# Performance work log

Measured on AMD Instinct MI355X. Metric: run time of the kernel, lower is better.

Reference implementation:

```python
import jax, jax.numpy as jnp
import numpy as np

NUM_ITERATIONS = 3


def squash(t, axis=-1):
    # scale * t / sqrt(||t||^2), scale = ||t||^2 / (1 + ||t||^2)
    sq = jnp.sum(t * t, axis=axis, keepdims=True)
    return t * (sq / ((1.0 + sq) * jnp.sqrt(sq)))


def setup_inputs() -> dict:
    key = jax.random.key(0)
    k1, k2 = jax.random.split(key)
    B, I, D = 512, 1152, 8   # batch, in_capsules, in_dim
    O, E = 10, 16            # out_capsules, out_dim
    x = jax.random.normal(k1, (B, I, D), dtype=jnp.float32)
    route_weights = jax.random.normal(k2, (O, I, D, E), dtype=jnp.float32)
    return {"x": x, "route_weights": route_weights}


def reference(x, route_weights):
    # priors: [O, B, I, E]  (torch version carries an extra singleton dim 3,
    # which only broadcasts; math is identical)
    priors = jnp.einsum('bid,oide->obie', x, route_weights)
    # logits broadcast over out_dim in the torch code (delta has keepdim=1 on
    # the last axis), so a [O, B, I, 1] logit tensor is exactly equivalent.
    logits = jnp.zeros(priors.shape[:3] + (1,), dtype=priors.dtype)
    outputs = None
    for it in range(NUM_ITERATIONS):
        probs = jax.nn.softmax(logits, axis=2)            # over in_capsules
        s = jnp.sum(probs * priors, axis=2, keepdims=True)  # [O, B, 1, E]
        outputs = squash(s, axis=-1)
        if it != NUM_ITERATIONS - 1:
            delta = jnp.sum(priors * outputs, axis=-1, keepdims=True)  # [O,B,I,1]
            logits = logits + delta
    # match torch output shape [out_capsules, batch, 1, 1, out_dim]
    return outputs[:, :, :, None, :]
```

## Files before the change

kernel.cpp:

```cpp
#include <hip/hip_runtime.h>

#define BATCH 512
#define NI 1152
#define ND 8
#define NO 10
#define NE 16

constexpr int THREADS = 512;
constexpr int WAVES   = THREADS / 64;
constexpr int QUADS   = THREADS / 4;
constexpr int ITEMS   = NI / QUADS;
constexpr int BB      = 2;
constexpr int BPG     = BATCH / BB;


__device__ __forceinline__ unsigned int bf16_rne(float f) {
    const unsigned int u = __builtin_bit_cast(unsigned int, f);
    return (u + 0x7fffu + ((u >> 16) & 1u)) >> 16;
}
__device__ __forceinline__ float bf_lo(unsigned int u) {
    return __builtin_bit_cast(float, u << 16);
}
__device__ __forceinline__ float bf_hi(unsigned int u) {
    return __builtin_bit_cast(float, u & 0xffff0000u);
}

__global__ __launch_bounds__(THREADS, 4)
void caps_routing(const float* __restrict__ x,
                  const float* __restrict__ Wt,
                  float* __restrict__ out)
{
    const int o  = blockIdx.x / BPG;
    const int b0 = (blockIdx.x % BPG) * BB;

    __shared__ __align__(16) unsigned int pl[BB][NI][NE / 2];
    __shared__ __align__(16) float red[BB][WAVES * 16];
    __shared__ float sv[BB][16];
    __shared__ float rsum[BB][WAVES];

    const int t    = threadIdx.x;
    const int lane = t & 63;
    const int w    = t >> 6;
    const int e4   = t & 3;
    const int iq   = t >> 2;

    const float* xb = x  + (size_t)b0 * (NI * ND);
    const float* Wo = Wt + (size_t)o * ((size_t)NI * ND * NE);

    float lg[BB][ITEMS];
    float4 acc[BB];
#pragma unroll
    for (int bb = 0; bb < BB; ++bb) acc[bb] = make_float4(0.f, 0.f, 0.f, 0.f);

#pragma unroll
    for (int k = 0; k < ITEMS; ++k) {
        const int i = iq + k * QUADS;
        float4 xa[BB], xc[BB];
#pragma unroll
        for (int bb = 0; bb < BB; ++bb) {
            const float* xr = xb + (size_t)bb * (NI * ND) + (size_t)i * ND;
            xa[bb] = *(const float4*)(xr);
            xc[bb] = *(const float4*)(xr + 4);
        }
        const float4* Wp = (const float4*)(Wo + (size_t)i * (ND * NE));
        float4 v[BB];
#pragma unroll
        for (int bb = 0; bb < BB; ++bb) v[bb] = make_float4(0.f, 0.f, 0.f, 0.f);
#define DSTEP(dd, FIELD, ARR) { const float4 wv = Wp[(dd)*4 + e4]; \
        _Pragma("unroll") \
        for (int bb = 0; bb < BB; ++bb) { const float xs = ARR[bb].FIELD; \
            v[bb].x += xs*wv.x; v[bb].y += xs*wv.y; \
            v[bb].z += xs*wv.z; v[bb].w += xs*wv.w; } }
        DSTEP(0, x, xa) DSTEP(1, y, xa) DSTEP(2, z, xa) DSTEP(3, w, xa)
        DSTEP(4, x, xc) DSTEP(5, y, xc) DSTEP(6, z, xc) DSTEP(7, w, xc)
#undef DSTEP
#pragma unroll
        for (int bb = 0; bb < BB; ++bb) {
            uint2 pk;
            pk.x = bf16_rne(v[bb].x) | (bf16_rne(v[bb].y) << 16);
            pk.y = bf16_rne(v[bb].z) | (bf16_rne(v[bb].w) << 16);
            *(uint2*)&pl[bb][i][e4 * 2] = pk;
            acc[bb].x += v[bb].x; acc[bb].y += v[bb].y;
            acc[bb].z += v[bb].z; acc[bb].w += v[bb].w;
        }
    }

#pragma unroll
    for (int bb = 0; bb < BB; ++bb) {
#pragma unroll
        for (int off = 4; off <= 32; off <<= 1) {
            acc[bb].x += __shfl_xor(acc[bb].x, off);
            acc[bb].y += __shfl_xor(acc[bb].y, off);
            acc[bb].z += __shfl_xor(acc[bb].z, off);
            acc[bb].w += __shfl_xor(acc[bb].w, off);
        }
        if (lane < 4) *(float4*)&red[bb][w * 16 + e4 * 4] = acc[bb];
    }
    __syncthreads();
    if (t < 16 * BB) {
        const int bb = t >> 4, e = t & 15;
        float s = 0.f;
#pragma unroll
        for (int q = 0; q < WAVES; ++q) s += red[bb][q * 16 + e];
        sv[bb][e] = s * (1.0f / (float)NI);
    }
    __syncthreads();

    float4 outv[BB];
#pragma unroll
    for (int bb = 0; bb < BB; ++bb) {
        float sq = 0.f;
#pragma unroll
        for (int e = 0; e < 16; ++e) { const float vv = sv[bb][e]; sq += vv * vv; }
        const float scale = sqrtf(sq) / (1.0f + sq);
        outv[bb].x = sv[bb][e4 * 4 + 0] * scale;
        outv[bb].y = sv[bb][e4 * 4 + 1] * scale;
        outv[bb].z = sv[bb][e4 * 4 + 2] * scale;
        outv[bb].w = sv[bb][e4 * 4 + 3] * scale;
    }

    for (int it = 1; it < 3; ++it) {
#pragma unroll
        for (int bb = 0; bb < BB; ++bb) {
            float4 pacc = make_float4(0.f, 0.f, 0.f, 0.f);
            float  lsum = 0.f;
#pragma unroll
            for (int k = 0; k < ITEMS; ++k) {
                const int i = iq + k * QUADS;
                const uint2 pk = *(const uint2*)&pl[bb][i][e4 * 2];
                const float vx = bf_lo(pk.x), vy = bf_hi(pk.x);
                const float vz = bf_lo(pk.y), vw = bf_hi(pk.y);
                float part = vx * outv[bb].x + vy * outv[bb].y
                           + vz * outv[bb].z + vw * outv[bb].w;
                part += __shfl_xor(part, 1);
                part += __shfl_xor(part, 2);
                const float l = (it == 1) ? part : (lg[bb][k] + part);
                lg[bb][k] = l;
                const float wgt = __expf(l);
                pacc.x += wgt * vx; pacc.y += wgt * vy;
                pacc.z += wgt * vz; pacc.w += wgt * vw;
                lsum += wgt;
            }
#pragma unroll
            for (int off = 4; off <= 32; off <<= 1) {
                pacc.x += __shfl_xor(pacc.x, off);
                pacc.y += __shfl_xor(pacc.y, off);
                pacc.z += __shfl_xor(pacc.z, off);
                pacc.w += __shfl_xor(pacc.w, off);
                lsum   += __shfl_xor(lsum, off);
            }
            if (lane < 4) *(float4*)&red[bb][w * 16 + e4 * 4] = pacc;
            if (lane == 0) rsum[bb][w] = lsum;
        }
        __syncthreads();
        if (t < 16 * BB) {
            const int bb = t >> 4, e = t & 15;
            float s = 0.f;
#pragma unroll
            for (int q = 0; q < WAVES; ++q) s += red[bb][q * 16 + e];
            float L = 0.f;
#pragma unroll
            for (int q = 0; q < WAVES; ++q) L += rsum[bb][q];
            sv[bb][e] = s / L;
        }
        __syncthreads();

        if (it == 1) {
#pragma unroll
            for (int bb = 0; bb < BB; ++bb) {
                float sq = 0.f;
#pragma unroll
                for (int e = 0; e < 16; ++e) { const float vv = sv[bb][e]; sq += vv * vv; }
                const float scale = sqrtf(sq) / (1.0f + sq);
                outv[bb].x = sv[bb][e4 * 4 + 0] * scale;
                outv[bb].y = sv[bb][e4 * 4 + 1] * scale;
                outv[bb].z = sv[bb][e4 * 4 + 2] * scale;
                outv[bb].w = sv[bb][e4 * 4 + 3] * scale;
            }
        }
    }

    if (t < 16 * BB) {
        const int bb = t >> 4, e = t & 15;
        float sq = 0.f;
#pragma unroll
        for (int ee = 0; ee < 16; ++ee) { const float vv = sv[bb][ee]; sq += vv * vv; }
        const float scale = sqrtf(sq) / (1.0f + sq);
        out[((size_t)o * BATCH + b0 + bb) * NE + e] = sv[bb][e] * scale;
    }
}

extern "C" void kernel_launch(void* const* d_in, const int* in_sizes, int n_in,
                              void* d_out, int out_size, void* d_ws, size_t ws_size,
                              hipStream_t stream) {
    const float* x  = (const float*)d_in[0];
    const float* Wt = (const float*)d_in[1];
    float* outp = (float*)d_out;
    caps_routing<<<dim3(NO * BPG), dim3(THREADS), 0, stream>>>(x, Wt, outp);
}
```

Measured before the change: 167.5 us.

## Split prior computation into separate kernel writing bf16 priors to workspace

Adds a caps_priors kernel that computes the priors once per 4-batch group, so weight loads are reused across four batches, and writes them as packed bf16 to global workspace. The routing kernel then copies its slice into shared memory and recomputes the first-iteration mean from the bf16 values. The aim is to cut the weight-load and FMA cost that the fused kernel paid with only two batches per block. In exchange it adds a global round trip of about 188 MB of bf16 priors and a second launch. The first-iteration sum now uses rounded priors instead of fp32 ones, and the old fused kernel is kept as a fallback when the workspace is too small.

```diff
diff --git a/kernel.cpp b/kernel.cpp
--- a/kernel.cpp
+++ b/kernel.cpp
@@ -5,6 +5,65 @@
 #define ND 8
 #define NO 10
 #define NE 16
+
+__device__ __forceinline__ unsigned int bf16_rne(float f) {
+    const unsigned int u = __builtin_bit_cast(unsigned int, f);
+    return (u + 0x7fffu + ((u >> 16) & 1u)) >> 16;
+}
+__device__ __forceinline__ float bf_lo(unsigned int u) {
+    return __builtin_bit_cast(float, u << 16);
+}
+__device__ __forceinline__ float bf_hi(unsigned int u) {
+    return __builtin_bit_cast(float, u & 0xffff0000u);
+}
+
+
+constexpr int A_THREADS = 512;
+constexpr int A_BB      = 4;
+constexpr int A_BPG     = BATCH / A_BB;
+constexpr int A_QUADS   = A_THREADS / 4;
+constexpr int A_ITEMS   = NI / A_QUADS;
+
+__global__ __launch_bounds__(A_THREADS, 8)
+void caps_priors(const float* __restrict__ x,
+                 const float* __restrict__ Wt,
+                 unsigned int* __restrict__ pws)
+{
+    const int o  = blockIdx.x / A_BPG;
+    const int b0 = (blockIdx.x % A_BPG) * A_BB;
+    const int t  = threadIdx.x;
+    const int e4 = t & 3;
+    const int iq = t >> 2;
+
+    const float* xb = x  + (size_t)b0 * (NI * ND);
+    const float* Wo = Wt + (size_t)o * ((size_t)NI * ND * NE);
+
+#pragma unroll
+    for (int k = 0; k < A_ITEMS; ++k) {
+        const int i = iq + k * A_QUADS;
+        const float4* Wp = (const float4*)(Wo + (size_t)i * (ND * NE));
+        float4 wv[8];
+#pragma unroll
+        for (int dd = 0; dd < 8; ++dd) wv[dd] = Wp[dd * 4 + e4];
+#pragma unroll
+        for (int bb = 0; bb < A_BB; ++bb) {
+            const float* xr = xb + (size_t)bb * (NI * ND) + (size_t)i * ND;
+            const float4 xa = *(const float4*)(xr);
+            const float4 xc = *(const float4*)(xr + 4);
+            float4 v = make_float4(0.f, 0.f, 0.f, 0.f);
+#define AD(dd, xs) { v.x += (xs)*wv[dd].x; v.y += (xs)*wv[dd].y; \
+                     v.z += (xs)*wv[dd].z; v.w += (xs)*wv[dd].w; }
+            AD(0, xa.x) AD(1, xa.y) AD(2, xa.z) AD(3, xa.w)
+            AD(4, xc.x) AD(5, xc.y) AD(6, xc.z) AD(7, xc.w)
+#undef AD
+            uint2 pk;
+            pk.x = bf16_rne(v.x) | (bf16_rne(v.y) << 16);
+            pk.y = bf16_rne(v.z) | (bf16_rne(v.w) << 16);
+            *(uint2*)(pws + (((size_t)o * BATCH + b0 + bb) * NI + i) * 8
+                          + e4 * 2) = pk;
+        }
+    }
+}
 
 constexpr int THREADS = 512;
 constexpr int WAVES   = THREADS / 64;
@@ -13,22 +72,9 @@
 constexpr int BB      = 2;
 constexpr int BPG     = BATCH / BB;
 
-
-__device__ __forceinline__ unsigned int bf16_rne(float f) {
-    const unsigned int u = __builtin_bit_cast(unsigned int, f);
-    return (u + 0x7fffu + ((u >> 16) & 1u)) >> 16;
-}
-__device__ __forceinline__ float bf_lo(unsigned int u) {
-    return __builtin_bit_cast(float, u << 16);
-}
-__device__ __forceinline__ float bf_hi(unsigned int u) {
-    return __builtin_bit_cast(float, u & 0xffff0000u);
-}
-
 __global__ __launch_bounds__(THREADS, 4)
-void caps_routing(const float* __restrict__ x,
-                  const float* __restrict__ Wt,
-                  float* __restrict__ out)
+void caps_routing2(const unsigned int* __restrict__ pws,
+                   float* __restrict__ out)
 {
     const int o  = blockIdx.x / BPG;
     const int b0 = (blockIdx.x % BPG) * BB;
@@ -44,49 +90,26 @@
     const int e4   = t & 3;
     const int iq   = t >> 2;
 
-    const float* xb = x  + (size_t)b0 * (NI * ND);
-    const float* Wo = Wt + (size_t)o * ((size_t)NI * ND * NE);
-
-    float lg[BB][ITEMS];
+    {
+        const uint4* src = (const uint4*)(pws + ((size_t)o * BATCH + b0) * NI * 8);
+        uint4* dst = (uint4*)&pl[0][0][0];
+#pragma unroll
+        for (int j = 0; j < (BB * NI * (NE / 2) / 4) / THREADS; ++j)
+            dst[t + j * THREADS] = src[t + j * THREADS];
+    }
+    __syncthreads();
+
     float4 acc[BB];
 #pragma unroll
     for (int bb = 0; bb < BB; ++bb) acc[bb] = make_float4(0.f, 0.f, 0.f, 0.f);
-
-#pragma unroll
-    for (int k = 0; k < ITEMS; ++k) {
-        const int i = iq + k * QUADS;
-        float4 xa[BB], xc[BB];
-#pragma unroll
-        for (int bb = 0; bb < BB; ++bb) {
-            const float* xr = xb + (size_t)bb * (NI * ND) + (size_t)i * ND;
-            xa[bb] = *(const float4*)(xr);
-            xc[bb] = *(const float4*)(xr + 4);
-        }
-        const float4* Wp = (const float4*)(Wo + (size_t)i * (ND * NE));
-        float4 v[BB];
-#pragma unroll
-        for (int bb = 0; bb < BB; ++bb) v[bb] = make_float4(0.f, 0.f, 0.f, 0.f);
-#define DSTEP(dd, FIELD, ARR) { const float4 wv = Wp[(dd)*4 + e4]; \
-        _Pragma("unroll") \
-        for (int bb = 0; bb < BB; ++bb) { const float xs = ARR[bb].FIELD; \
-            v[bb].x += xs*wv.x; v[bb].y += xs*wv.y; \
-            v[bb].z += xs*wv.z; v[bb].w += xs*wv.w; } }
-        DSTEP(0, x, xa) DSTEP(1, y, xa) DSTEP(2, z, xa) DSTEP(3, w, xa)
-        DSTEP(4, x, xc) DSTEP(5, y, xc) DSTEP(6, z, xc) DSTEP(7, w, xc)
-#undef DSTEP
-#pragma unroll
-        for (int bb = 0; bb < BB; ++bb) {
-            uint2 pk;
-            pk.x = bf16_rne(v[bb].x) | (bf16_rne(v[bb].y) << 16);
-            pk.y = bf16_rne(v[bb].z) | (bf16_rne(v[bb].w) << 16);
-            *(uint2*)&pl[bb][i][e4 * 2] = pk;
-            acc[bb].x += v[bb].x; acc[bb].y += v[bb].y;
-            acc[bb].z += v[bb].z; acc[bb].w += v[bb].w;
-        }
-    }
-
 #pragma unroll
     for (int bb = 0; bb < BB; ++bb) {
+#pragma unroll
+        for (int k = 0; k < ITEMS; ++k) {
+            const uint2 pk = *(const uint2*)&pl[bb][iq + k * QUADS][e4 * 2];
+            acc[bb].x += bf_lo(pk.x); acc[bb].y += bf_hi(pk.x);
+            acc[bb].z += bf_lo(pk.y); acc[bb].w += bf_hi(pk.y);
+        }
 #pragma unroll
         for (int off = 4; off <= 32; off <<= 1) {
             acc[bb].x += __shfl_xor(acc[bb].x, off);
@@ -119,6 +142,7 @@
         outv[bb].w = sv[bb][e4 * 4 + 3] * scale;
     }
 
+    float lg[BB][ITEMS];
     for (int it = 1; it < 3; ++it) {
 #pragma unroll
         for (int bb = 0; bb < BB; ++bb) {
@@ -126,8 +150,7 @@
             float  lsum = 0.f;
 #pragma unroll
             for (int k = 0; k < ITEMS; ++k) {
-                const int i = iq + k * QUADS;
-                const uint2 pk = *(const uint2*)&pl[bb][i][e4 * 2];
+                const uint2 pk = *(const uint2*)&pl[bb][iq + k * QUADS][e4 * 2];
                 const float vx = bf_lo(pk.x), vy = bf_hi(pk.x);
                 const float vz = bf_lo(pk.y), vw = bf_hi(pk.y);
                 float part = vx * outv[bb].x + vy * outv[bb].y
@@ -190,11 +213,183 @@
     }
 }
 
+__global__ __launch_bounds__(THREADS, 4)
+void caps_routing_fb(const float* __restrict__ x,
+                     const float* __restrict__ Wt,
+                     float* __restrict__ out)
+{
+    const int o  = blockIdx.x / BPG;
+    const int b0 = (blockIdx.x % BPG) * BB;
+
+    __shared__ __align__(16) unsigned int pl[BB][NI][NE / 2];
+    __shared__ __align__(16) float red[BB][WAVES * 16];
+    __shared__ float sv[BB][16];
+    __shared__ float rsum[BB][WAVES];
+
+    const int t    = threadIdx.x;
+    const int lane = t & 63;
+    const int w    = t >> 6;
+    const int e4   = t & 3;
+    const int iq   = t >> 2;
+
+    const float* xb = x  + (size_t)b0 * (NI * ND);
+    const float* Wo = Wt + (size_t)o * ((size_t)NI * ND * NE);
+
+    float lg[BB][ITEMS];
+    float4 acc[BB];
+#pragma unroll
+    for (int bb = 0; bb < BB; ++bb) acc[bb] = make_float4(0.f, 0.f, 0.f, 0.f);
+
+#pragma unroll
+    for (int k = 0; k < ITEMS; ++k) {
+        const int i = iq + k * QUADS;
+        float4 xa[BB], xc[BB];
+#pragma unroll
+        for (int bb = 0; bb < BB; ++bb) {
+            const float* xr = xb + (size_t)bb * (NI * ND) + (size_t)i * ND;
+            xa[bb] = *(const float4*)(xr);
+            xc[bb] = *(const float4*)(xr + 4);
+        }
+        const float4* Wp = (const float4*)(Wo + (size_t)i * (ND * NE));
+        float4 v[BB];
+#pragma unroll
+        for (int bb = 0; bb < BB; ++bb) v[bb] = make_float4(0.f, 0.f, 0.f, 0.f);
+#define DSTEP(dd, FIELD, ARR) { const float4 wv = Wp[(dd)*4 + e4]; \
+        _Pragma("unroll") \
+        for (int bb = 0; bb < BB; ++bb) { const float xs = ARR[bb].FIELD; \
+            v[bb].x += xs*wv.x; v[bb].y += xs*wv.y; \
+            v[bb].z += xs*wv.z; v[bb].w += xs*wv.w; } }
+        DSTEP(0, x, xa) DSTEP(1, y, xa) DSTEP(2, z, xa) DSTEP(3, w, xa)
+        DSTEP(4, x, xc) DSTEP(5, y, xc) DSTEP(6, z, xc) DSTEP(7, w, xc)
+#undef DSTEP
+#pragma unroll
+        for (int bb = 0; bb < BB; ++bb) {
+            uint2 pk;
+            pk.x = bf16_rne(v[bb].x) | (bf16_rne(v[bb].y) << 16);
+            pk.y = bf16_rne(v[bb].z) | (bf16_rne(v[bb].w) << 16);
+            *(uint2*)&pl[bb][i][e4 * 2] = pk;
+            acc[bb].x += v[bb].x; acc[bb].y += v[bb].y;
+            acc[bb].z += v[bb].z; acc[bb].w += v[bb].w;
+        }
+    }
+
+#pragma unroll
+    for (int bb = 0; bb < BB; ++bb) {
+#pragma unroll
+        for (int off = 4; off <= 32; off <<= 1) {
+            acc[bb].x += __shfl_xor(acc[bb].x, off);
+            acc[bb].y += __shfl_xor(acc[bb].y, off);
+            acc[bb].z += __shfl_xor(acc[bb].z, off);
+            acc[bb].w += __shfl_xor(acc[bb].w, off);
+        }
+        if (lane < 4) *(float4*)&red[bb][w * 16 + e4 * 4] = acc[bb];
+    }
+    __syncthreads();
+    if (t < 16 * BB) {
+        const int bb = t >> 4, e = t & 15;
+        float s = 0.f;
+#pragma unroll
+        for (int q = 0; q < WAVES; ++q) s += red[bb][q * 16 + e];
+        sv[bb][e] = s * (1.0f / (float)NI);
+    }
+    __syncthreads();
+
+    float4 outv[BB];
+#pragma unroll
+    for (int bb = 0; bb < BB; ++bb) {
+        float sq = 0.f;
+#pragma unroll
+        for (int e = 0; e < 16; ++e) { const float vv = sv[bb][e]; sq += vv * vv; }
+        const float scale = sqrtf(sq) / (1.0f + sq);
+        outv[bb].x = sv[bb][e4 * 4 + 0] * scale;
+        outv[bb].y = sv[bb][e4 * 4 + 1] * scale;
+        outv[bb].z = sv[bb][e4 * 4 + 2] * scale;
+        outv[bb].w = sv[bb][e4 * 4 + 3] * scale;
+    }
+
+    for (int it = 1; it < 3; ++it) {
+#pragma unroll
+        for (int bb = 0; bb < BB; ++bb) {
+            float4 pacc = make_float4(0.f, 0.f, 0.f, 0.f);
+            float  lsum = 0.f;
+#pragma unroll
+            for (int k = 0; k < ITEMS; ++k) {
+                const uint2 pk = *(const uint2*)&pl[bb][iq + k * QUADS][e4 * 2];
+                const float vx = bf_lo(pk.x), vy = bf_hi(pk.x);
+                const float vz = bf_lo(pk.y), vw = bf_hi(pk.y);
+                float part = vx * outv[bb].x + vy * outv[bb].y
+                           + vz * outv[bb].z + vw * outv[bb].w;
+                part += __shfl_xor(part, 1);
+                part += __shfl_xor(part, 2);
+                const float l = (it == 1) ? part : (lg[bb][k] + part);
+                lg[bb][k] = l;
+                const float wgt = __expf(l);
+                pacc.x += wgt * vx; pacc.y += wgt * vy;
+                pacc.z += wgt * vz; pacc.w += wgt * vw;
+                lsum += wgt;
+            }
+#pragma unroll
+            for (int off = 4; off <= 32; off <<= 1) {
+                pacc.x += __shfl_xor(pacc.x, off);
+                pacc.y += __shfl_xor(pacc.y, off);
+                pacc.z += __shfl_xor(pacc.z, off);
+                pacc.w += __shfl_xor(pacc.w, off);
+                lsum   += __shfl_xor(lsum, off);
+            }
+            if (lane < 4) *(float4*)&red[bb][w * 16 + e4 * 4] = pacc;
+            if (lane == 0) rsum[bb][w] = lsum;
+        }
+        __syncthreads();
+        if (t < 16 * BB) {
+            const int bb = t >> 4, e = t & 15;
+            float s = 0.f;
+#pragma unroll
+            for (int q = 0; q < WAVES; ++q) s += red[bb][q * 16 + e];
+            float L = 0.f;
+#pragma unroll
+            for (int q = 0; q < WAVES; ++q) L += rsum[bb][q];
+            sv[bb][e] = s / L;
+        }
+        __syncthreads();
+
+        if (it == 1) {
+#pragma unroll
+            for (int bb = 0; bb < BB; ++bb) {
+                float sq = 0.f;
+#pragma unroll
+                for (int e = 0; e < 16; ++e) { const float vv = sv[bb][e]; sq += vv * vv; }
+                const float scale = sqrtf(sq) / (1.0f + sq);
+                outv[bb].x = sv[bb][e4 * 4 + 0] * scale;
+                outv[bb].y = sv[bb][e4 * 4 + 1] * scale;
+                outv[bb].z = sv[bb][e4 * 4 + 2] * scale;
+                outv[bb].w = sv[bb][e4 * 4 + 3] * scale;
+            }
+        }
+    }
+
+    if (t < 16 * BB) {
+        const int bb = t >> 4, e = t & 15;
+        float sq = 0.f;
+#pragma unroll
+        for (int ee = 0; ee < 16; ++ee) { const float vv = sv[bb][ee]; sq += vv * vv; }
+        const float scale = sqrtf(sq) / (1.0f + sq);
+        out[((size_t)o * BATCH + b0 + bb) * NE + e] = sv[bb][e] * scale;
+    }
+}
+
 extern "C" void kernel_launch(void* const* d_in, const int* in_sizes, int n_in,
                               void* d_out, int out_size, void* d_ws, size_t ws_size,
                               hipStream_t stream) {
     const float* x  = (const float*)d_in[0];
     const float* Wt = (const float*)d_in[1];
     float* outp = (float*)d_out;
-    caps_routing<<<dim3(NO * BPG), dim3(THREADS), 0, stream>>>(x, Wt, outp);
-}
+
+    const size_t need = (size_t)NO * BATCH * NI * (NE / 2) * sizeof(unsigned int);
+    if (ws_size >= need) {
+        unsigned int* pws = (unsigned int*)d_ws;
+        caps_priors<<<dim3(NO * A_BPG), dim3(A_THREADS), 0, stream>>>(x, Wt, pws);
+        caps_routing2<<<dim3(NO * BPG), dim3(THREADS), 0, stream>>>(pws, outp);
+    } else {
+        caps_routing_fb<<<dim3(NO * BPG), dim3(THREADS), 0, stream>>>(x, Wt, outp);
+    }
+}
```

Measured after the change: 213.5 us. +27.5%, slower.
